# Kernel tuning notes

Measured on AMD Instinct MI355X. Metric: run time of the kernel, lower is better.

The kernel has to match this reference:

```python
import jax, jax.numpy as jnp
import numpy as np

EPS = 1e-8  # torch CosineSimilarity default eps
MARGIN = 0.1


def _normalize(x):
    # row-normalize with eps clamp on the norm (matches torch cosine_similarity)
    n = jnp.sqrt(jnp.sum(x * x, axis=-1, keepdims=True))
    return x / jnp.maximum(n, EPS)


def setup_inputs() -> dict:
    key = jax.random.key(0)
    k1, k2, k3 = jax.random.split(key, 3)
    B, D, C = 1024, 512, 100000
    inputs = jax.random.normal(k1, (B, D), dtype=jnp.float32)
    class_embeddings = jax.random.normal(k2, (C, D), dtype=jnp.float32)
    targets = jax.random.randint(k3, (B,), 0, C, dtype=jnp.int64)
    return {"inputs": inputs, "class_embeddings": class_embeddings, "targets": targets}


def reference(inputs, class_embeddings, targets):
    B = inputs.shape[0]
    x_n = _normalize(inputs)                    # [B, D]
    c_n = _normalize(class_embeddings)          # [C, D]
    # cosine similarity against ALL classes: the repeat/expand in the original
    # is just this normalized matmul.
    scores = jnp.einsum('bd,cd->bc', x_n, c_n)  # [B, C]
    # cosine similarity with the target class embedding
    target_cos = scores[jnp.arange(B), targets]  # [B]
    hinge = jnp.maximum(0.0, MARGIN - target_cos[:, None] + scores)  # [B, C]
    per_sample = jnp.sum(hinge, axis=1) - MARGIN  # subtract the target's own margin term
    return jnp.mean(per_sample)
```

## Files before the change

### kernel.cpp

```cpp
#include <hip/hip_runtime.h>
#include <stdint.h>

#define NB 1024
#define ND 512
#define NC 100000
#define MTILES 391
#define MARGINF 0.1f

using bf16x8 = __attribute__((ext_vector_type(8))) short;
using f32x4  = __attribute__((ext_vector_type(4))) float;

__device__ __forceinline__ uint32_t f2bf(float f) {
  uint32_t u = __float_as_uint(f);
  return (u + 0x7fffu + ((u >> 16) & 1u)) >> 16;
}
__device__ __forceinline__ uint32_t pack2bf(float x, float y) {
  return f2bf(x) | (f2bf(y) << 16);
}

__global__ __launch_bounds__(256)
void normalize_relayout(const float* __restrict__ src, uint16_t* __restrict__ dst) {
  __shared__ uint16_t lds[16][520];
  const int lane = threadIdx.x & 63;
  const int wv = threadIdx.x >> 6;
  const size_t R0 = (size_t)blockIdx.x << 4;
  #pragma unroll
  for (int i = 0; i < 4; ++i) {
    const int r = (wv << 2) + i;
    const float4* s = (const float4*)(src + (R0 + r) * ND) + (lane << 1);
    float4 a = s[0], b = s[1];
    float ss = a.x*a.x + a.y*a.y + a.z*a.z + a.w*a.w
             + b.x*b.x + b.y*b.y + b.z*b.z + b.w*b.w;
    #pragma unroll
    for (int o = 32; o; o >>= 1) ss += __shfl_xor(ss, o);
    const float inv = 1.0f / fmaxf(sqrtf(ss), 1e-8f);
    uint4 o4;
    o4.x = pack2bf(a.x * inv, a.y * inv);
    o4.y = pack2bf(a.z * inv, a.w * inv);
    o4.z = pack2bf(b.x * inv, b.y * inv);
    o4.w = pack2bf(b.z * inv, b.w * inv);
    *(uint4*)(&lds[r][lane << 3]) = o4;
  }
  __syncthreads();
  uint16_t* out = dst + ((size_t)blockIdx.x << 13);
  #pragma unroll
  for (int c = 0; c < 4; ++c) {
    const int idx = (c << 8) + threadIdx.x;
    const int kc = idx >> 6, g = (idx >> 4) & 3, rs = idx & 15;
    uint4 v = *(const uint4*)(&lds[rs][(kc << 5) + (g << 3)]);
    ((uint4*)out)[idx] = v;
  }
}

__global__ void target_cos_kernel(const float* __restrict__ x,
                                  const float* __restrict__ cls,
                                  const int* __restrict__ tgt,
                                  float* __restrict__ t) {
  const int b = blockIdx.x;
  const int row = tgt[b];
  const float2* xr = (const float2*)(x + (size_t)b * ND);
  const float2* cr = (const float2*)(cls + (size_t)row * ND);
  float2 xv = xr[threadIdx.x], cv = cr[threadIdx.x];
  float sx = xv.x * xv.x + xv.y * xv.y;
  float sc = cv.x * cv.x + cv.y * cv.y;
  float sd = xv.x * cv.x + xv.y * cv.y;
  #pragma unroll
  for (int o = 32; o; o >>= 1) {
    sx += __shfl_down(sx, o);
    sc += __shfl_down(sc, o);
    sd += __shfl_down(sd, o);
  }
  __shared__ float r[3][4];
  const int wv = threadIdx.x >> 6;
  if ((threadIdx.x & 63) == 0) { r[0][wv] = sx; r[1][wv] = sc; r[2][wv] = sd; }
  __syncthreads();
  if (threadIdx.x == 0) {
    float ax = r[0][0] + r[0][1] + r[0][2] + r[0][3];
    float ac = r[1][0] + r[1][1] + r[1][2] + r[1][3];
    float ad = r[2][0] + r[2][1] + r[2][2] + r[2][3];
    t[b] = ad / (fmaxf(sqrtf(ax), 1e-8f) * fmaxf(sqrtf(ac), 1e-8f));
  }
}

__device__ __forceinline__ void gload16(const char* g, char* l) {
  __builtin_amdgcn_global_load_lds(
      (__attribute__((address_space(1))) void*)(g),
      (__attribute__((address_space(3))) void*)(l), 16, 0, 0);
}
#define WAITVM(N)  asm volatile("s_waitcnt vmcnt(" #N ")" ::: "memory")
#define LGKM0()    asm volatile("s_waitcnt lgkmcnt(0)" ::: "memory")
#define MEMFENCE() asm volatile("" ::: "memory")

__global__ __launch_bounds__(512, 2)
void hinge_gemm_pipe(const uint16_t* __restrict__ Wf,
                     const uint16_t* __restrict__ Xf,
                     const float* __restrict__ t,
                     float* __restrict__ accum) {
  const int id = blockIdx.x;
  const int mt = (id & 7) + ((id >> 5) << 3);
  const int nt = (id >> 3) & 3;
  if (mt >= MTILES) return;

  __shared__ __align__(1024) char lds[131072];
  __shared__ float part[8];

  const int lane = threadIdx.x & 63;
  const int wv = threadIdx.x >> 6;
  const int wm = wv & 1;
  const int wn = wv >> 1;
  const int laneoff = lane << 4;
  const int aoff = wm << 13;
  const int boff = (1 << 14) + (wn << 12);

  const char* gsrc[4];
  int dsto[4];
  #pragma unroll
  for (int i = 0; i < 4; ++i) {
    const int sl = (wv << 2) + i;
    if (sl < 16) {
      gsrc[i] = (const char*)Wf + (((size_t)(mt * 16 + sl)) << 14) + laneoff;
      dsto[i] = sl << 10;
    } else {
      gsrc[i] = (const char*)Xf + (((size_t)(nt * 16 + (sl - 16))) << 14) + laneoff;
      dsto[i] = (1 << 14) + ((sl - 16) << 10);
    }
  }

  f32x4 acc[8][4];
  #pragma unroll
  for (int i = 0; i < 8; ++i)
    #pragma unroll
    for (int j = 0; j < 4; ++j)
      acc[i][j] = (f32x4){0.f, 0.f, 0.f, 0.f};

#define STAGE(T) {                                                         \
    char* lb_ = lds + (((T) & 3) << 15);                                   \
    _Pragma("unroll")                                                      \
    for (int i_ = 0; i_ < 4; ++i_)                                         \
      gload16(gsrc[i_] + ((size_t)(T) << 10), lb_ + dsto[i_]);             \
  }

#define COMPUTE(KT) {                                                      \
    const char* base_ = lds + (((KT) & 3) << 15);                          \
    bf16x8 a_[8]; bf16x8 b_[4];                                            \
    _Pragma("unroll")                                                      \
    for (int ms_ = 0; ms_ < 8; ++ms_)                                      \
      a_[ms_] = *(const bf16x8*)(base_ + aoff + (ms_ << 10) + laneoff);    \
    _Pragma("unroll")                                                      \
    for (int j_ = 0; j_ < 4; ++j_)                                         \
      b_[j_] = *(const bf16x8*)(base_ + boff + (j_ << 10) + laneoff);      \
    LGKM0();                                                               \
    __builtin_amdgcn_sched_barrier(0);                                     \
    __builtin_amdgcn_s_barrier();   \
    __builtin_amdgcn_s_setprio(1);                                         \
    _Pragma("unroll")                                                      \
    for (int ms_ = 0; ms_ < 8; ++ms_)                                      \
      _Pragma("unroll")                                                    \
      for (int j_ = 0; j_ < 4; ++j_)                                       \
        acc[ms_][j_] = __builtin_amdgcn_mfma_f32_16x16x32_bf16(            \
            a_[ms_], b_[j_], acc[ms_][j_], 0, 0, 0);                       \
    __builtin_amdgcn_s_setprio(0);                                         \
  }

  STAGE(0); STAGE(1); STAGE(2);

  #pragma unroll 1
  for (int kt = 0; kt < 13; ++kt) {
    STAGE(kt + 3);
    WAITVM(12);
    __builtin_amdgcn_s_barrier();
    MEMFENCE();
    COMPUTE(kt);
  }
  WAITVM(8);  __builtin_amdgcn_s_barrier(); MEMFENCE(); COMPUTE(13);
  WAITVM(4);  __builtin_amdgcn_s_barrier(); MEMFENCE(); COMPUTE(14);
  WAITVM(0);  __builtin_amdgcn_s_barrier(); MEMFENCE(); COMPUTE(15);

  const int m0 = mt << 8, n0 = nt << 8;
  const int lr = lane & 15;
  const int rb4 = (lane >> 4) << 2;
  float local = 0.f;
  #pragma unroll
  for (int j = 0; j < 4; ++j) {
    const int n = n0 + (wn << 6) + (j << 4) + lr;
    const float base = MARGINF - t[n];
    #pragma unroll
    for (int ms = 0; ms < 8; ++ms) {
      const int mr = m0 + (wm << 7) + (ms << 4) + rb4;
      f32x4 v = acc[ms][j];
      #pragma unroll
      for (int rr = 0; rr < 4; ++rr)
        if (mr + rr < NC) local += fmaxf(base + v[rr], 0.f);
    }
  }
  #pragma unroll
  for (int o = 32; o; o >>= 1) local += __shfl_down(local, o);
  if (lane == 0) part[wv] = local;
  __syncthreads();
  if (threadIdx.x == 0) {
    float s = 0.f;
    #pragma unroll
    for (int i = 0; i < 8; ++i) s += part[i];
    atomicAdd(&accum[id & 63], s);
  }
#undef STAGE
#undef COMPUTE
}

__global__ void finalize_kernel(const float* __restrict__ accum, float* __restrict__ out) {
  float s = 0.f;
  #pragma unroll
  for (int i = 0; i < 64; ++i) s += accum[i];
  out[0] = s * (1.0f / (float)NB) - MARGINF;
}

#define WS_WF 0
#define WS_XF 102400000ull
#define WS_T  103448576ull
#define WS_ACC 103452672ull

extern "C" void kernel_launch(void* const* d_in, const int* in_sizes, int n_in,
                              void* d_out, int out_size, void* d_ws, size_t ws_size,
                              hipStream_t stream) {
  const float* inputs = (const float*)d_in[0];
  const float* cls    = (const float*)d_in[1];
  const int*   tgt    = (const int*)d_in[2];
  float* out = (float*)d_out;
  char* ws = (char*)d_ws;
  uint16_t* Wf = (uint16_t*)(ws + WS_WF);
  uint16_t* Xf = (uint16_t*)(ws + WS_XF);
  float* t     = (float*)(ws + WS_T);
  float* accum = (float*)(ws + WS_ACC);

  (void)hipMemsetAsync(accum, 0, 64 * sizeof(float), stream);
  normalize_relayout<<<64, 256, 0, stream>>>(inputs, Xf);
  normalize_relayout<<<6250, 256, 0, stream>>>(cls, Wf);
  target_cos_kernel<<<NB, 256, 0, stream>>>(inputs, cls, tgt, t);
  hinge_gemm_pipe<<<1568, 512, 0, stream>>>(Wf, Xf, t, accum);
  finalize_kernel<<<1, 1, 0, stream>>>(accum, out);
}
```

Measured before the change: 426.9 us.

## Split GEMM k-step into half-stages interleaving global loads, LDS reads and MFMAs

Each k-iteration of the bf16 hinge GEMM is split into two halves. Each half issues half of the next stage's global-to-LDS loads, reads only the A/B fragments it needs, then runs 16 MFMAs, so global loads, LDS reads and matrix math overlap more finely. Iterations now use one workgroup barrier instead of two, with the vmcnt wait moved just before the second MFMA group. In exchange the A fragments need more register state, and the synchronization is more delicate and must still protect ring-buffer reuse.

```diff
diff --git a/kernel.cpp b/kernel.cpp
--- a/kernel.cpp
+++ b/kernel.cpp
@@ -89,7 +89,6 @@
 }
 #define WAITVM(N)  asm volatile("s_waitcnt vmcnt(" #N ")" ::: "memory")
 #define LGKM0()    asm volatile("s_waitcnt lgkmcnt(0)" ::: "memory")
-#define MEMFENCE() asm volatile("" ::: "memory")
 
 __global__ __launch_bounds__(512, 2)
 void hinge_gemm_pipe(const uint16_t* __restrict__ Wf,
@@ -133,48 +132,77 @@
     for (int j = 0; j < 4; ++j)
       acc[i][j] = (f32x4){0.f, 0.f, 0.f, 0.f};
 
-#define STAGE(T) {                                                         \
+  bf16x8 a03[4], a47[4], bfr[4];
+
+#define STAGE_H(T, H) {                                                    \
     char* lb_ = lds + (((T) & 3) << 15);                                   \
+    gload16(gsrc[(H)*2]     + ((size_t)(T) << 10), lb_ + dsto[(H)*2]);     \
+    gload16(gsrc[(H)*2 + 1] + ((size_t)(T) << 10), lb_ + dsto[(H)*2 + 1]); }
+
+#define DSR_A03B(KT) {                                                     \
+    const char* base_ = lds + (((KT) & 3) << 15);                          \
     _Pragma("unroll")                                                      \
     for (int i_ = 0; i_ < 4; ++i_)                                         \
-      gload16(gsrc[i_] + ((size_t)(T) << 10), lb_ + dsto[i_]);             \
-  }
-
-#define COMPUTE(KT) {                                                      \
+      a03[i_] = *(const bf16x8*)(base_ + aoff + (i_ << 10) + laneoff);     \
+    _Pragma("unroll")                                                      \
+    for (int j_ = 0; j_ < 4; ++j_)                                         \
+      bfr[j_] = *(const bf16x8*)(base_ + boff + (j_ << 10) + laneoff); }
+
+#define DSR_A47(KT) {                                                      \
     const char* base_ = lds + (((KT) & 3) << 15);                          \
-    bf16x8 a_[8]; bf16x8 b_[4];                                            \
-    _Pragma("unroll")                                                      \
-    for (int ms_ = 0; ms_ < 8; ++ms_)                                      \
-      a_[ms_] = *(const bf16x8*)(base_ + aoff + (ms_ << 10) + laneoff);    \
-    _Pragma("unroll")                                                      \
-    for (int j_ = 0; j_ < 4; ++j_)                                         \
-      b_[j_] = *(const bf16x8*)(base_ + boff + (j_ << 10) + laneoff);      \
-    LGKM0();                                                               \
-    __builtin_amdgcn_sched_barrier(0);                                     \
-    __builtin_amdgcn_s_barrier();   \
+    _Pragma("unroll")                                                      \
+    for (int i_ = 0; i_ < 4; ++i_)                                         \
+      a47[i_] = *(const bf16x8*)(base_ + aoff + ((i_ + 4) << 10) + laneoff); }
+
+#define MFMA_LO() {                                                        \
     __builtin_amdgcn_s_setprio(1);                                         \
     _Pragma("unroll")                                                      \
-    for (int ms_ = 0; ms_ < 8; ++ms_)                                      \
+    for (int m_ = 0; m_ < 4; ++m_)                                         \
       _Pragma("unroll")                                                    \
       for (int j_ = 0; j_ < 4; ++j_)                                       \
-        acc[ms_][j_] = __builtin_amdgcn_mfma_f32_16x16x32_bf16(            \
-            a_[ms_], b_[j_], acc[ms_][j_], 0, 0, 0);                       \
-    __builtin_amdgcn_s_setprio(0);                                         \
-  }
-
-  STAGE(0); STAGE(1); STAGE(2);
+        acc[m_][j_] = __builtin_amdgcn_mfma_f32_16x16x32_bf16(             \
+            a03[m_], bfr[j_], acc[m_][j_], 0, 0, 0);                       \
+    __builtin_amdgcn_s_setprio(0); }
+
+#define MFMA_HI() {                                                        \
+    __builtin_amdgcn_s_setprio(1);                                         \
+    _Pragma("unroll")                                                      \
+    for (int m_ = 0; m_ < 4; ++m_)                                         \
+      _Pragma("unroll")                                                    \
+      for (int j_ = 0; j_ < 4; ++j_)                                       \
+        acc[m_ + 4][j_] = __builtin_amdgcn_mfma_f32_16x16x32_bf16(         \
+            a47[m_], bfr[j_], acc[m_ + 4][j_], 0, 0, 0);                   \
+    __builtin_amdgcn_s_setprio(0); }
+
+  STAGE_H(0, 0); STAGE_H(0, 1);
+  STAGE_H(1, 0); STAGE_H(1, 1);
+  STAGE_H(2, 0); STAGE_H(2, 1);
+  WAITVM(8);
+  __builtin_amdgcn_s_barrier();
 
   #pragma unroll 1
   for (int kt = 0; kt < 13; ++kt) {
-    STAGE(kt + 3);
-    WAITVM(12);
+    STAGE_H(kt + 3, 0);
+    DSR_A03B(kt);
+    LGKM0();
+    __builtin_amdgcn_sched_barrier(0);
+    MFMA_LO();
+    STAGE_H(kt + 3, 1);
+    DSR_A47(kt);
+    WAITVM(8);
+    LGKM0();
+    __builtin_amdgcn_sched_barrier(0);
+    MFMA_HI();
     __builtin_amdgcn_s_barrier();
-    MEMFENCE();
-    COMPUTE(kt);
-  }
-  WAITVM(8);  __builtin_amdgcn_s_barrier(); MEMFENCE(); COMPUTE(13);
-  WAITVM(4);  __builtin_amdgcn_s_barrier(); MEMFENCE(); COMPUTE(14);
-  WAITVM(0);  __builtin_amdgcn_s_barrier(); MEMFENCE(); COMPUTE(15);
+  }
+  DSR_A03B(13); LGKM0(); __builtin_amdgcn_sched_barrier(0); MFMA_LO();
+  DSR_A47(13);  WAITVM(4); LGKM0(); __builtin_amdgcn_sched_barrier(0); MFMA_HI();
+  __builtin_amdgcn_s_barrier();
+  DSR_A03B(14); LGKM0(); __builtin_amdgcn_sched_barrier(0); MFMA_LO();
+  DSR_A47(14);  WAITVM(0); LGKM0(); __builtin_amdgcn_sched_barrier(0); MFMA_HI();
+  __builtin_amdgcn_s_barrier();
+  DSR_A03B(15); LGKM0(); __builtin_amdgcn_sched_barrier(0); MFMA_LO();
+  DSR_A47(15);  LGKM0(); __builtin_amdgcn_sched_barrier(0); MFMA_HI();
 
   const int m0 = mt << 8, n0 = nt << 8;
   const int lr = lane & 15;
@@ -203,8 +231,11 @@
     for (int i = 0; i < 8; ++i) s += part[i];
     atomicAdd(&accum[id & 63], s);
   }
-#undef STAGE
-#undef COMPUTE
+#undef STAGE_H
+#undef DSR_A03B
+#undef DSR_A47
+#undef MFMA_LO
+#undef MFMA_HI
 }
 
 __global__ void finalize_kernel(const float* __restrict__ accum, float* __restrict__ out) {
```

After: 446.5 us. 1.05x slower.

## Load GEMM B operand directly into registers and split compute into half-tiles

Applied to the files above, without the earlier changes.

The X (B) operand no longer goes through LDS. It is loaded from global memory straight into double-buffered registers one k-step ahead, which halves LDS use to 64KB and leaves only the class-embedding A tiles staged through LDS. Each k-tile's MFMA work is split into two halves with interleaved LDS reads, global-to-LDS staging and barriers, to overlap memory traffic with matrix math. The cost is more barriers per tile, extra VGPRs for the B buffers, and reliance on compiler-inserted waits for the register loads.

```diff
diff --git a/kernel.cpp b/kernel.cpp
--- a/kernel.cpp
+++ b/kernel.cpp
@@ -89,7 +89,6 @@
 }
 #define WAITVM(N)  asm volatile("s_waitcnt vmcnt(" #N ")" ::: "memory")
 #define LGKM0()    asm volatile("s_waitcnt lgkmcnt(0)" ::: "memory")
-#define MEMFENCE() asm volatile("" ::: "memory")
 
 __global__ __launch_bounds__(512, 2)
 void hinge_gemm_pipe(const uint16_t* __restrict__ Wf,
@@ -101,7 +100,7 @@
   const int nt = (id >> 3) & 3;
   if (mt >= MTILES) return;
 
-  __shared__ __align__(1024) char lds[131072];
+  __shared__ __align__(1024) char lds[65536];
   __shared__ float part[8];
 
   const int lane = threadIdx.x & 63;
@@ -110,21 +109,16 @@
   const int wn = wv >> 1;
   const int laneoff = lane << 4;
   const int aoff = wm << 13;
-  const int boff = (1 << 14) + (wn << 12);
-
-  const char* gsrc[4];
-  int dsto[4];
-  #pragma unroll
-  for (int i = 0; i < 4; ++i) {
-    const int sl = (wv << 2) + i;
-    if (sl < 16) {
-      gsrc[i] = (const char*)Wf + (((size_t)(mt * 16 + sl)) << 14) + laneoff;
-      dsto[i] = sl << 10;
-    } else {
-      gsrc[i] = (const char*)Xf + (((size_t)(nt * 16 + (sl - 16))) << 14) + laneoff;
-      dsto[i] = (1 << 14) + ((sl - 16) << 10);
-    }
-  }
+
+  const char* gA0 = (const char*)Wf + (((size_t)(mt * 16 + wv * 2)) << 14) + laneoff;
+  const char* gA1 = gA0 + (1 << 14);
+  const int d0 = (wv * 2) << 10;
+  const int d1 = d0 + 1024;
+
+  const char* bp0 = (const char*)Xf + (((size_t)(nt * 16 + wn * 4 + 0)) << 14) + laneoff;
+  const char* bp1 = (const char*)Xf + (((size_t)(nt * 16 + wn * 4 + 1)) << 14) + laneoff;
+  const char* bp2 = (const char*)Xf + (((size_t)(nt * 16 + wn * 4 + 2)) << 14) + laneoff;
+  const char* bp3 = (const char*)Xf + (((size_t)(nt * 16 + wn * 4 + 3)) << 14) + laneoff;
 
   f32x4 acc[8][4];
   #pragma unroll
@@ -133,48 +127,86 @@
     for (int j = 0; j < 4; ++j)
       acc[i][j] = (f32x4){0.f, 0.f, 0.f, 0.f};
 
+  bf16x8 a_[4];
+  bf16x8 bA[4], bB[4];
+
 #define STAGE(T) {                                                         \
-    char* lb_ = lds + (((T) & 3) << 15);                                   \
+    char* lb_ = lds + (((T) & 3) << 14);                                   \
+    gload16(gA0 + ((size_t)(T) << 10), lb_ + d0);                          \
+    gload16(gA1 + ((size_t)(T) << 10), lb_ + d1); }
+
+#define BLOAD(T, R) {                                                      \
+    R[0] = *(const bf16x8*)(bp0 + ((size_t)(T) << 10));                    \
+    R[1] = *(const bf16x8*)(bp1 + ((size_t)(T) << 10));                    \
+    R[2] = *(const bf16x8*)(bp2 + ((size_t)(T) << 10));                    \
+    R[3] = *(const bf16x8*)(bp3 + ((size_t)(T) << 10)); }
+
+#define DSR_LO(KT) {                                                       \
+    const char* b_ = lds + (((KT) & 3) << 14) + aoff + laneoff;            \
+    a_[0] = *(const bf16x8*)(b_);                                          \
+    a_[1] = *(const bf16x8*)(b_ + 1024);                                   \
+    a_[2] = *(const bf16x8*)(b_ + 2048);                                   \
+    a_[3] = *(const bf16x8*)(b_ + 3072); }
+
+#define DSR_HI(KT) {                                                       \
+    const char* b_ = lds + (((KT) & 3) << 14) + aoff + laneoff;            \
+    a_[0] = *(const bf16x8*)(b_ + 4096);                                   \
+    a_[1] = *(const bf16x8*)(b_ + 5120);                                   \
+    a_[2] = *(const bf16x8*)(b_ + 6144);                                   \
+    a_[3] = *(const bf16x8*)(b_ + 7168); }
+
+#define MFMA_LO(BR) {                                                      \
+    __builtin_amdgcn_s_setprio(1);                                         \
     _Pragma("unroll")                                                      \
-    for (int i_ = 0; i_ < 4; ++i_)                                         \
-      gload16(gsrc[i_] + ((size_t)(T) << 10), lb_ + dsto[i_]);             \
-  }
-
-#define COMPUTE(KT) {                                                      \
-    const char* base_ = lds + (((KT) & 3) << 15);                          \
-    bf16x8 a_[8]; bf16x8 b_[4];                                            \
+    for (int m_ = 0; m_ < 4; ++m_)                                         \
+      _Pragma("unroll")                                                    \
+      for (int j_ = 0; j_ < 4; ++j_)                                       \
+        acc[m_][j_] = __builtin_amdgcn_mfma_f32_16x16x32_bf16(             \
+            a_[m_], BR[j_], acc[m_][j_], 0, 0, 0);                         \
+    __builtin_amdgcn_s_setprio(0); }
+
+#define MFMA_HI(BR) {                                                      \
+    __builtin_amdgcn_s_setprio(1);                                         \
     _Pragma("unroll")                                                      \
-    for (int ms_ = 0; ms_ < 8; ++ms_)                                      \
-      a_[ms_] = *(const bf16x8*)(base_ + aoff + (ms_ << 10) + laneoff);    \
-    _Pragma("unroll")                                                      \
-    for (int j_ = 0; j_ < 4; ++j_)                                         \
-      b_[j_] = *(const bf16x8*)(base_ + boff + (j_ << 10) + laneoff);      \
+    for (int m_ = 0; m_ < 4; ++m_)                                         \
+      _Pragma("unroll")                                                    \
+      for (int j_ = 0; j_ < 4; ++j_)                                       \
+        acc[m_ + 4][j_] = __builtin_amdgcn_mfma_f32_16x16x32_bf16(         \
+            a_[m_], BR[j_], acc[m_ + 4][j_], 0, 0, 0);                     \
+    __builtin_amdgcn_s_setprio(0); }
+
+#define TILE(KT, CURB, NXTB, DOSTAGE, DOBLOAD, VMN) {                      \
+    DSR_LO(KT);                                                            \
+    if (DOBLOAD) BLOAD((KT) + 1, NXTB);                                    \
+    if (DOSTAGE) STAGE((KT) + 3);                                          \
+    __builtin_amdgcn_s_barrier();                                          \
     LGKM0();                                                               \
     __builtin_amdgcn_sched_barrier(0);                                     \
-    __builtin_amdgcn_s_barrier();   \
-    __builtin_amdgcn_s_setprio(1);                                         \
-    _Pragma("unroll")                                                      \
-    for (int ms_ = 0; ms_ < 8; ++ms_)                                      \
-      _Pragma("unroll")                                                    \
-      for (int j_ = 0; j_ < 4; ++j_)                                       \
-        acc[ms_][j_] = __builtin_amdgcn_mfma_f32_16x16x32_bf16(            \
-            a_[ms_], b_[j_], acc[ms_][j_], 0, 0, 0);                       \
-    __builtin_amdgcn_s_setprio(0);                                         \
-  }
-
+    MFMA_LO(CURB);                                                         \
+    __builtin_amdgcn_s_barrier();                                          \
+    DSR_HI(KT);                                                            \
+    WAITVM(VMN);                                                           \
+    __builtin_amdgcn_s_barrier();                                          \
+    LGKM0();                                                               \
+    __builtin_amdgcn_sched_barrier(0);                                     \
+    MFMA_HI(CURB);                                                         \
+    __builtin_amdgcn_s_barrier(); }
+
+  BLOAD(0, bA);
   STAGE(0); STAGE(1); STAGE(2);
+  WAITVM(4);
+  __builtin_amdgcn_s_barrier();
 
   #pragma unroll 1
-  for (int kt = 0; kt < 13; ++kt) {
-    STAGE(kt + 3);
-    WAITVM(12);
-    __builtin_amdgcn_s_barrier();
-    MEMFENCE();
-    COMPUTE(kt);
-  }
-  WAITVM(8);  __builtin_amdgcn_s_barrier(); MEMFENCE(); COMPUTE(13);
-  WAITVM(4);  __builtin_amdgcn_s_barrier(); MEMFENCE(); COMPUTE(14);
-  WAITVM(0);  __builtin_amdgcn_s_barrier(); MEMFENCE(); COMPUTE(15);
+  for (int tt = 0; tt < 6; ++tt) {
+    const int kt = tt << 1;
+    TILE(kt,     bA, bB, 1, 1, 8);
+    TILE(kt + 1, bB, bA, 1, 1, 8);
+  }
+  TILE(12, bA, bB, 1, 1, 8);
+  TILE(13, bB, bA, 0, 1, 8);
+  TILE(14, bA, bB, 0, 1, 8);
+  TILE(15, bB, bA, 0, 0, 0);
 
   const int m0 = mt << 8, n0 = nt << 8;
   const int lr = lane & 15;
@@ -204,7 +236,12 @@
     atomicAdd(&accum[id & 63], s);
   }
 #undef STAGE
-#undef COMPUTE
+#undef BLOAD
+#undef DSR_LO
+#undef DSR_HI
+#undef MFMA_LO
+#undef MFMA_HI
+#undef TILE
 }
 
 __global__ void finalize_kernel(const float* __restrict__ accum, float* __restrict__ out) {
```

New measurement: 426.6 us. Within noise of the previous version (-0.1%).

## Software-pipeline LDS fragment loads with MFMA and fuse prep/finalize launches

Applied to the files above, without the earlier changes.

The GEMM main loop now double-buffers B fragments in registers and splits the A fragments into two halves. The next tile's LDS reads are issued while the current tile's MFMAs run, and the barrier is placed mid-tile. Each wave stages four contiguous slices with a single base pointer. The memset, the small-input normalize and the target-cosine kernels are merged into one prep launch, and the finalize kernel is replaced by a last-block-done atomic counter inside the GEMM. This cuts launch overhead and LDS latency stalls, at the cost of more registers and a threadfence/atomic per block.

```diff
diff --git a/kernel.cpp b/kernel.cpp
--- a/kernel.cpp
+++ b/kernel.cpp
@@ -5,6 +5,7 @@
 #define ND 512
 #define NC 100000
 #define MTILES 391
+#define NBLK 1568
 #define MARGINF 0.1f
 
 using bf16x8 = __attribute__((ext_vector_type(8))) short;
@@ -18,12 +19,13 @@
   return f2bf(x) | (f2bf(y) << 16);
 }
 
-__global__ __launch_bounds__(256)
-void normalize_relayout(const float* __restrict__ src, uint16_t* __restrict__ dst) {
+__device__ __forceinline__ void normalize_body(const float* __restrict__ src,
+                                               uint16_t* __restrict__ dst,
+                                               int blk) {
   __shared__ uint16_t lds[16][520];
   const int lane = threadIdx.x & 63;
   const int wv = threadIdx.x >> 6;
-  const size_t R0 = (size_t)blockIdx.x << 4;
+  const size_t R0 = (size_t)blk << 4;
   #pragma unroll
   for (int i = 0; i < 4; ++i) {
     const int r = (wv << 2) + i;
@@ -42,7 +44,7 @@
     *(uint4*)(&lds[r][lane << 3]) = o4;
   }
   __syncthreads();
-  uint16_t* out = dst + ((size_t)blockIdx.x << 13);
+  uint16_t* out = dst + ((size_t)blk << 13);
   #pragma unroll
   for (int c = 0; c < 4; ++c) {
     const int idx = (c << 8) + threadIdx.x;
@@ -52,11 +54,15 @@
   }
 }
 
-__global__ void target_cos_kernel(const float* __restrict__ x,
-                                  const float* __restrict__ cls,
-                                  const int* __restrict__ tgt,
-                                  float* __restrict__ t) {
-  const int b = blockIdx.x;
+__global__ __launch_bounds__(256)
+void normalize_relayout(const float* __restrict__ src, uint16_t* __restrict__ dst) {
+  normalize_body(src, dst, blockIdx.x);
+}
+
+__device__ __forceinline__ void tcos_body(const float* __restrict__ x,
+                                          const float* __restrict__ cls,
+                                          const int* __restrict__ tgt,
+                                          float* __restrict__ t, int b) {
   const int row = tgt[b];
   const float2* xr = (const float2*)(x + (size_t)b * ND);
   const float2* cr = (const float2*)(cls + (size_t)row * ND);
@@ -82,27 +88,43 @@
   }
 }
 
+__global__ __launch_bounds__(256)
+void prep_kernel(const float* __restrict__ inputs, const float* __restrict__ cls,
+                 const int* __restrict__ tgt, uint16_t* __restrict__ Xf,
+                 float* __restrict__ t, float* __restrict__ accum) {
+  const int bid = blockIdx.x;
+  if (bid < 64) {
+    normalize_body(inputs, Xf, bid);
+  } else if (bid < 64 + NB) {
+    tcos_body(inputs, cls, tgt, t, bid - 64);
+  } else {
+    if (threadIdx.x < 64) accum[threadIdx.x] = 0.0f;
+  }
+}
+
 __device__ __forceinline__ void gload16(const char* g, char* l) {
   __builtin_amdgcn_global_load_lds(
       (__attribute__((address_space(1))) void*)(g),
       (__attribute__((address_space(3))) void*)(l), 16, 0, 0);
 }
 #define WAITVM(N)  asm volatile("s_waitcnt vmcnt(" #N ")" ::: "memory")
-#define LGKM0()    asm volatile("s_waitcnt lgkmcnt(0)" ::: "memory")
-#define MEMFENCE() asm volatile("" ::: "memory")
+#define LGKM(N)    asm volatile("s_waitcnt lgkmcnt(" #N ")" ::: "memory")
+#define SBAR()     __builtin_amdgcn_sched_barrier(0)
 
 __global__ __launch_bounds__(512, 2)
 void hinge_gemm_pipe(const uint16_t* __restrict__ Wf,
                      const uint16_t* __restrict__ Xf,
                      const float* __restrict__ t,
-                     float* __restrict__ accum) {
+                     float* __restrict__ accum,
+                     float* __restrict__ outp) {
   const int id = blockIdx.x;
   const int mt = (id & 7) + ((id >> 5) << 3);
   const int nt = (id >> 3) & 3;
-  if (mt >= MTILES) return;
+  unsigned* ctr = (unsigned*)(accum + 63);
 
   __shared__ __align__(1024) char lds[131072];
   __shared__ float part[8];
+  __shared__ bool lastf;
 
   const int lane = threadIdx.x & 63;
   const int wv = threadIdx.x >> 6;
@@ -112,18 +134,29 @@
   const int aoff = wm << 13;
   const int boff = (1 << 14) + (wn << 12);
 
-  const char* gsrc[4];
-  int dsto[4];
-  #pragma unroll
-  for (int i = 0; i < 4; ++i) {
-    const int sl = (wv << 2) + i;
-    if (sl < 16) {
-      gsrc[i] = (const char*)Wf + (((size_t)(mt * 16 + sl)) << 14) + laneoff;
-      dsto[i] = sl << 10;
-    } else {
-      gsrc[i] = (const char*)Xf + (((size_t)(nt * 16 + (sl - 16))) << 14) + laneoff;
-      dsto[i] = (1 << 14) + ((sl - 16) << 10);
+  auto epilogue_mark = [&]() {
+    __threadfence();
+    if (threadIdx.x == 0) lastf = (atomicAdd(ctr, 1u) == (unsigned)(NBLK - 1));
+    __syncthreads();
+    if (lastf) {
+      float v = 0.f;
+      if (threadIdx.x < 32) v = atomicAdd(&accum[threadIdx.x], 0.0f);
+      #pragma unroll
+      for (int o = 32; o; o >>= 1) v += __shfl_down(v, o);
+      if (threadIdx.x == 0) outp[0] = v * (1.0f / (float)NB) - MARGINF;
     }
+  };
+
+  if (mt >= MTILES) { epilogue_mark(); return; }
+
+  const char* gstage;
+  int dstage;
+  if (wv < 4) {
+    gstage = (const char*)Wf + (((size_t)(mt * 16 + wv * 4)) << 14) + laneoff;
+    dstage = (wv * 4) << 10;
+  } else {
+    gstage = (const char*)Xf + (((size_t)(nt * 16 + (wv - 4) * 4)) << 14) + laneoff;
+    dstage = (1 << 14) + (((wv - 4) * 4) << 10);
   }
 
   f32x4 acc[8][4];
@@ -133,48 +166,100 @@
     for (int j = 0; j < 4; ++j)
       acc[i][j] = (f32x4){0.f, 0.f, 0.f, 0.f};
 
+  bf16x8 a03[4], a47[4], bA[4], bB[4];
+
 #define STAGE(T) {                                                         \
-    char* lb_ = lds + (((T) & 3) << 15);                                   \
-    _Pragma("unroll")                                                      \
-    for (int i_ = 0; i_ < 4; ++i_)                                         \
-      gload16(gsrc[i_] + ((size_t)(T) << 10), lb_ + dsto[i_]);             \
-  }
-
-#define COMPUTE(KT) {                                                      \
-    const char* base_ = lds + (((KT) & 3) << 15);                          \
-    bf16x8 a_[8]; bf16x8 b_[4];                                            \
-    _Pragma("unroll")                                                      \
-    for (int ms_ = 0; ms_ < 8; ++ms_)                                      \
-      a_[ms_] = *(const bf16x8*)(base_ + aoff + (ms_ << 10) + laneoff);    \
-    _Pragma("unroll")                                                      \
-    for (int j_ = 0; j_ < 4; ++j_)                                         \
-      b_[j_] = *(const bf16x8*)(base_ + boff + (j_ << 10) + laneoff);      \
-    LGKM0();                                                               \
-    __builtin_amdgcn_sched_barrier(0);                                     \
-    __builtin_amdgcn_s_barrier();   \
+    char* lb_ = lds + (((T) & 3) << 15) + dstage;                          \
+    const char* g_ = gstage + ((size_t)(T) << 10);                         \
+    gload16(g_,          lb_);                                             \
+    gload16(g_ + 16384,  lb_ + 1024);                                      \
+    gload16(g_ + 32768,  lb_ + 2048);                                      \
+    gload16(g_ + 49152,  lb_ + 3072); }
+
+#define ISSUE_A03(KT) {                                                    \
+    const char* b_ = lds + (((KT) & 3) << 15) + aoff + laneoff;            \
+    a03[0] = *(const bf16x8*)(b_);                                         \
+    a03[1] = *(const bf16x8*)(b_ + 1024);                                  \
+    a03[2] = *(const bf16x8*)(b_ + 2048);                                  \
+    a03[3] = *(const bf16x8*)(b_ + 3072); }
+
+#define ISSUE_A47(KT) {                                                    \
+    const char* b_ = lds + (((KT) & 3) << 15) + aoff + laneoff;            \
+    a47[0] = *(const bf16x8*)(b_ + 4096);                                  \
+    a47[1] = *(const bf16x8*)(b_ + 5120);                                  \
+    a47[2] = *(const bf16x8*)(b_ + 6144);                                  \
+    a47[3] = *(const bf16x8*)(b_ + 7168); }
+
+#define ISSUE_B(KT, BR) {                                                  \
+    const char* b_ = lds + (((KT) & 3) << 15) + boff + laneoff;            \
+    BR[0] = *(const bf16x8*)(b_);                                          \
+    BR[1] = *(const bf16x8*)(b_ + 1024);                                   \
+    BR[2] = *(const bf16x8*)(b_ + 2048);                                   \
+    BR[3] = *(const bf16x8*)(b_ + 3072); }
+
+#define MFMA_LO(BR) {                                                      \
     __builtin_amdgcn_s_setprio(1);                                         \
     _Pragma("unroll")                                                      \
-    for (int ms_ = 0; ms_ < 8; ++ms_)                                      \
+    for (int m_ = 0; m_ < 4; ++m_)                                         \
       _Pragma("unroll")                                                    \
       for (int j_ = 0; j_ < 4; ++j_)                                       \
-        acc[ms_][j_] = __builtin_amdgcn_mfma_f32_16x16x32_bf16(            \
-            a_[ms_], b_[j_], acc[ms_][j_], 0, 0, 0);                       \
-    __builtin_amdgcn_s_setprio(0);                                         \
-  }
+        acc[m_][j_] = __builtin_amdgcn_mfma_f32_16x16x32_bf16(             \
+            a03[m_], BR[j_], acc[m_][j_], 0, 0, 0);                        \
+    __builtin_amdgcn_s_setprio(0); }
+
+#define MFMA_HI(BR) {                                                      \
+    __builtin_amdgcn_s_setprio(1);                                         \
+    _Pragma("unroll")                                                      \
+    for (int m_ = 0; m_ < 4; ++m_)                                         \
+      _Pragma("unroll")                                                    \
+      for (int j_ = 0; j_ < 4; ++j_)                                       \
+        acc[m_ + 4][j_] = __builtin_amdgcn_mfma_f32_16x16x32_bf16(         \
+            a47[m_], BR[j_], acc[m_ + 4][j_], 0, 0, 0);                    \
+    __builtin_amdgcn_s_setprio(0); }
+
+#define TILE(KT, BP, BN, DOSTAGE, VMW) {                                   \
+    if (DOSTAGE) STAGE((KT) + 3);                                          \
+    ISSUE_A47(KT);                                                         \
+    SBAR();                                                                \
+    LGKM(4);                                                               \
+    SBAR();                                                                \
+    MFMA_LO(BP);                                                           \
+    VMW;                                                                   \
+    LGKM(0);                                                               \
+    SBAR();                                                                \
+    __builtin_amdgcn_s_barrier();                                          \
+    ISSUE_A03((KT) + 1);                                                   \
+    ISSUE_B((KT) + 1, BN);                                                 \
+    SBAR();                                                                \
+    MFMA_HI(BP); }
+
+#define TILE_LAST(KT, BP) {                                                \
+    ISSUE_A47(KT);                                                         \
+    SBAR();                                                                \
+    LGKM(4);                                                               \
+    SBAR();                                                                \
+    MFMA_LO(BP);                                                           \
+    LGKM(0);                                                               \
+    SBAR();                                                                \
+    MFMA_HI(BP); }
 
   STAGE(0); STAGE(1); STAGE(2);
+  WAITVM(8);
+  __builtin_amdgcn_s_barrier();
+  ISSUE_A03(0);
+  ISSUE_B(0, bA);
+  SBAR();
 
   #pragma unroll 1
-  for (int kt = 0; kt < 13; ++kt) {
-    STAGE(kt + 3);
-    WAITVM(12);
-    __builtin_amdgcn_s_barrier();
-    MEMFENCE();
-    COMPUTE(kt);
-  }
-  WAITVM(8);  __builtin_amdgcn_s_barrier(); MEMFENCE(); COMPUTE(13);
-  WAITVM(4);  __builtin_amdgcn_s_barrier(); MEMFENCE(); COMPUTE(14);
-  WAITVM(0);  __builtin_amdgcn_s_barrier(); MEMFENCE(); COMPUTE(15);
+  for (int tt = 0; tt < 6; ++tt) {
+    const int kt = tt << 1;
+    TILE(kt,     bA, bB, 1, WAITVM(8));
+    TILE(kt + 1, bB, bA, 1, WAITVM(8));
+  }
+  TILE(12, bA, bB, 1, WAITVM(8));
+  TILE(13, bB, bA, 0, WAITVM(4));
+  TILE(14, bA, bB, 0, WAITVM(0));
+  TILE_LAST(15, bB);
 
   const int m0 = mt << 8, n0 = nt << 8;
   const int lr = lane & 15;
@@ -201,17 +286,17 @@
     float s = 0.f;
     #pragma unroll
     for (int i = 0; i < 8; ++i) s += part[i];
-    atomicAdd(&accum[id & 63], s);
-  }
+    atomicAdd(&accum[id & 31], s);
+  }
+  epilogue_mark();
 #undef STAGE
-#undef COMPUTE
-}
-
-__global__ void finalize_kernel(const float* __restrict__ accum, float* __restrict__ out) {
-  float s = 0.f;
-  #pragma unroll
-  for (int i = 0; i < 64; ++i) s += accum[i];
-  out[0] = s * (1.0f / (float)NB) - MARGINF;
+#undef ISSUE_A03
+#undef ISSUE_A47
+#undef ISSUE_B
+#undef MFMA_LO
+#undef MFMA_HI
+#undef TILE
+#undef TILE_LAST
 }
 
 #define WS_WF 0
@@ -232,10 +317,7 @@
   float* t     = (float*)(ws + WS_T);
   float* accum = (float*)(ws + WS_ACC);
 
-  (void)hipMemsetAsync(accum, 0, 64 * sizeof(float), stream);
-  normalize_relayout<<<64, 256, 0, stream>>>(inputs, Xf);
+  prep_kernel<<<64 + NB + 1, 256, 0, stream>>>(inputs, cls, tgt, Xf, t, accum);
   normalize_relayout<<<6250, 256, 0, stream>>>(cls, Wf);
-  target_cos_kernel<<<NB, 256, 0, stream>>>(inputs, cls, tgt, t);
-  hinge_gemm_pipe<<<1568, 512, 0, stream>>>(Wf, Xf, t, accum);
-  finalize_kernel<<<1, 1, 0, stream>>>(accum, out);
-}
+  hinge_gemm_pipe<<<NBLK, 512, 0, stream>>>(Wf, Xf, t, accum, out);
+}
```

After: 610.2 us. +42.9%, slower.
